# Performance work log

Hardware: AMD Instinct MI355X
Metric: run time of the kernel (lower is better)

The kernel has to match this reference:

```python
import jax, jax.numpy as jnp
import numpy as np
from jax import lax

DN = ('NHWC', 'HWIO', 'NHWC')


def _conv(x, w):
    # x: [B,H,W,Cin], w: [kh,kw,Cin,Cout], 'same' padding
    return lax.conv_general_dilated(x, w, (1, 1), 'SAME', dimension_numbers=DN)


def _hard_sigmoid(x):
    # Keras hard_sigmoid: clip(0.2*x + 0.5, 0, 1)
    return jnp.clip(0.2 * x + 0.5, 0.0, 1.0)


def convlstm2d(x, Wk, Uk, b, filters):
    """Keras ConvLSTM2D, return_sequences=True, padding='same'.
    x: [B,T,H,W,Cin]. Gate order in kernel: [i, f, c, o].
    Returns h sequence [B,T,H,W,filters].
    """
    B, T, H, W, _ = x.shape
    h0 = jnp.zeros((B, H, W, filters), x.dtype)
    c0 = jnp.zeros((B, H, W, filters), x.dtype)

    def step(carry, xt):
        h, c = carry
        z = _conv(xt, Wk) + _conv(h, Uk) + b  # [B,H,W,4*filters]
        zi, zf, zc, zo = jnp.split(z, 4, axis=-1)
        i = _hard_sigmoid(zi)
        f = _hard_sigmoid(zf)
        o = _hard_sigmoid(zo)
        c_new = f * c + i * jnp.tanh(zc)
        h_new = o * jnp.tanh(c_new)
        return (h_new, c_new), h_new

    xs = jnp.moveaxis(x, 1, 0)  # [T,B,H,W,Cin]
    _, hs = lax.scan(step, (h0, c0), xs)
    return jnp.moveaxis(hs, 0, 1)  # [B,T,H,W,filters]


def setup_inputs() -> dict:
    key = jax.random.key(0)
    ks = jax.random.split(key, 7)
    B, T, H, W, Cin, F = 8, 10, 64, 64, 32, 64
    s = 0.05
    return {
        'x': jax.random.normal(ks[0], (B, T, H, W, Cin), jnp.float32),
        'Wk1': jax.random.normal(ks[1], (5, 5, Cin, 4 * F), jnp.float32) * s,
        'Uk1': jax.random.normal(ks[2], (5, 5, F, 4 * F), jnp.float32) * s,
        'b1': jnp.zeros((4 * F,), jnp.float32),
        'Wk2': jax.random.normal(ks[3], (3, 3, F, 4 * F), jnp.float32) * s,
        'Uk2': jax.random.normal(ks[4], (3, 3, F, 4 * F), jnp.float32) * s,
        'b2': jnp.zeros((4 * F,), jnp.float32),
    }


def reference(x, Wk1, Uk1, b1, Wk2, Uk2, b2):
    F = Uk1.shape[2]
    y = jax.nn.relu(convlstm2d(x, Wk1, Uk1, b1, F))
    y = jax.nn.relu(convlstm2d(y, Wk2, Uk2, b2, F))
    return y
```

## Files before the change

### kernel.cpp

```cpp
#include <hip/hip_runtime.h>
#include <cstdint>
#include <cmath>


#define NT        256
#define NTU       256

typedef __attribute__((ext_vector_type(8))) short short8;
typedef __attribute__((ext_vector_type(4))) float f32x4;

__device__ __forceinline__ float hsig(float v) {
    return fminf(fmaxf(fmaf(v, 0.2f, 0.5f), 0.0f), 1.0f);
}

__device__ __forceinline__ short bf16rnd(float f) {
    union { float f; unsigned u; } a; a.f = f;
    return (short)((a.u + 0x7FFFu + ((a.u >> 16) & 1u)) >> 16);
}

__device__ __forceinline__ void split_bf16(float f, short& h, short& l) {
    h = bf16rnd(f);
    union { unsigned u; float f; } b; b.u = ((unsigned)(unsigned short)h) << 16;
    l = bf16rnd(f - b.f);
}

__device__ __forceinline__ float from_bf16(short s) {
    union { unsigned u; float f; } b; b.u = ((unsigned)(unsigned short)s) << 16;
    return b.f;
}

struct BF { uint4 bh[4]; uint4 bl[4]; };

template<int CINX, int KS, bool WRITE_SEQ, bool HZ>
__device__ __forceinline__ void step_body(
    short* __restrict__ xs, short* __restrict__ hs,
    const short* __restrict__ xp, long xp_bstride,
    const short* __restrict__ h_prev,
    float* __restrict__ c_state,
    const short* __restrict__ Wpk,
    const short* __restrict__ Upk,
    const float* __restrict__ bias,
    short* __restrict__ h_next,
    short* __restrict__ seq, long seq_bstride,
    float* __restrict__ outf, long outf_bs,
    int bidx)
{
    constexpr int PAD  = KS / 2;
    constexpr int COLS = 64 + 2 * PAD;
    constexpr int CHX  = CINX / 32;
    constexpr int SEGS = HZ ? CHX : (CHX + 2);
    constexpr int PSTX = 2 * CINX + 8;
    constexpr int PSTH = 136;
    constexpr int VPPX = CINX / 4;

    const int tid  = threadIdx.x;
    const int lane = tid & 63;
    const int fg   = tid >> 6;
    const int q8   = ((lane >> 4) & 3) * 8;
    const int batch = bidx >> 6;
    const int y     = bidx & 63;

    const short* xim = xp + (size_t)batch * xp_bstride;
    const short* him = h_prev + (size_t)batch * 4096 * 128;

    for (int idx = tid; idx < (COLS * PSTX) / 8; idx += NT) {
        uint4 z; z.x = 0; z.y = 0; z.z = 0; z.w = 0;
        *(uint4*)(xs + idx * 8) = z;
    }
    if constexpr (!HZ) {
        for (int idx = tid; idx < (COLS * PSTH) / 8; idx += NT) {
            uint4 z; z.x = 0; z.y = 0; z.z = 0; z.w = 0;
            *(uint4*)(hs + idx * 8) = z;
        }
    }

    f32x4 acc[4][4];
    #pragma unroll
    for (int g = 0; g < 4; ++g)
        #pragma unroll
        for (int mt = 0; mt < 4; ++mt)
            #pragma unroll
            for (int r = 0; r < 4; ++r) acc[g][mt][r] = 0.0f;

    auto loadB = [&](int ky, int kx, int s) -> BF {
        int tap = ky * KS + kx;
        const short* base;
        if (s < CHX)
            base = Wpk + ((size_t)((tap * CHX + s) * 16 + fg)) * 1024 + lane * 16;
        else
            base = Upk + ((size_t)((tap * 2 + (s - CHX)) * 16 + fg)) * 1024 + lane * 16;
        BF b;
        #pragma unroll
        for (int g = 0; g < 4; ++g) {
            b.bh[g] = *(const uint4*)(base + (size_t)g * 4096);
            b.bl[g] = *(const uint4*)(base + (size_t)g * 4096 + 8);
        }
        return b;
    };

    const int ky0   = (y < PAD) ? (PAD - y) : 0;
    const int kyend = (64 + PAD - y) < KS ? (64 + PAD - y) : KS;

    BF bcur = loadB(ky0, 0, 0);

    for (int ky = ky0; ky < kyend; ++ky) {
        int yin = y + ky - PAD;
        __syncthreads();
        const short* xrow = xim + (size_t)yin * 64 * 2 * CINX;
        for (int idx = tid; idx < 64 * VPPX; idx += NT) {
            int px = idx / VPPX;
            int v  = idx - px * VPPX;
            *(uint4*)(xs + (px + PAD) * PSTX + v * 8)
                = *(const uint4*)(xrow + px * 2 * CINX + v * 8);
        }
        if constexpr (!HZ) {
            const short* hrow = him + (size_t)yin * 64 * 128;
            for (int idx = tid; idx < 64 * 16; idx += NT) {
                int px = idx >> 4;
                int v  = idx & 15;
                *(uint4*)(hs + (px + PAD) * PSTH + v * 8)
                    = *(const uint4*)(hrow + px * 128 + v * 8);
            }
        }
        __syncthreads();

        #pragma unroll
        for (int kx = 0; kx < KS; ++kx) {
            #pragma unroll
            for (int s = 0; s < SEGS; ++s) {
                int ns = s + 1, nkx = kx, nky = ky;
                if (ns == SEGS) { ns = 0; ++nkx; }
                if (nkx == KS)  { nkx = 0; ++nky; }
                nky = (nky < kyend) ? nky : ky;
                BF bnxt = loadB(nky, nkx, ns);

                short8 ah[4], al[4];
                #pragma unroll
                for (int mt = 0; mt < 4; ++mt) {
                    int col = mt * 16 + (lane & 15) + kx;
                    const short* p = (s < CHX)
                        ? (xs + col * PSTX + s * 32 + q8)
                        : (hs + col * PSTH + (s - CHX) * 32 + q8);
                    int lo = (s < CHX) ? CINX : 64;
                    ah[mt] = *(const short8*)p;
                    al[mt] = *(const short8*)(p + lo);
                }
                #pragma unroll
                for (int g = 0; g < 4; ++g) {
                    short8 bh = *(const short8*)&bcur.bh[g];
                    short8 bl = *(const short8*)&bcur.bl[g];
                    #pragma unroll
                    for (int mt = 0; mt < 4; ++mt) {
                        acc[g][mt] = __builtin_amdgcn_mfma_f32_16x16x32_bf16(
                            ah[mt], bh, acc[g][mt], 0, 0, 0);
                        acc[g][mt] = __builtin_amdgcn_mfma_f32_16x16x32_bf16(
                            al[mt], bh, acc[g][mt], 0, 0, 0);
                        acc[g][mt] = __builtin_amdgcn_mfma_f32_16x16x32_bf16(
                            ah[mt], bl, acc[g][mt], 0, 0, 0);
                    }
                }
                bcur = bnxt;
            }
        }
    }

    const int fl = fg * 16 + (lane & 15);
    const float b_i = bias[fl];
    const float b_f = bias[64 + fl];
    const float b_c = bias[128 + fl];
    const float b_o = bias[192 + fl];
    const int q = (lane >> 4) & 3;

    const long pixbase = (long)batch * 4096 + (long)y * 64;
    const long cb = pixbase * 64 + fl;
    const long sb = (long)batch * seq_bstride + ((long)y * 64) * 128 + fl;
    const long ob = (long)batch * outf_bs + ((long)y * 64) * 64 + fl;

    #pragma unroll
    for (int mt = 0; mt < 4; ++mt) {
        #pragma unroll
        for (int r = 0; r < 4; ++r) {
            int col = mt * 16 + q * 4 + r;
            long cidx = cb + (long)col * 64;
            float zi = acc[0][mt][r] + b_i;
            float zf = acc[1][mt][r] + b_f;
            float zc = acc[2][mt][r] + b_c;
            float zo = acc[3][mt][r] + b_o;
            float ig = hsig(zi);
            float fgt = hsig(zf);
            float og = hsig(zo);
            float cp = HZ ? 0.0f : c_state[cidx];
            float cn = fgt * cp + ig * tanhf(zc);
            float hn = og * tanhf(cn);
            c_state[cidx] = cn;

            if (h_next) {
                short hh, hl;
                split_bf16(hn, hh, hl);
                long hoff = (pixbase + col) * 128 + fl;
                h_next[hoff]      = hh;
                h_next[hoff + 64] = hl;
            }
            if (WRITE_SEQ) {
                short hh, hl;
                split_bf16(hn, hh, hl);
                bool pos = hn > 0.0f;
                seq[sb + (long)col * 128]      = pos ? hh : (short)0;
                seq[sb + (long)col * 128 + 64] = pos ? hl : (short)0;
            }
            if (outf)
                outf[ob + (long)col * 64] = fmaxf(hn, 0.0f);
        }
    }
}

template<int CINX, int KS, bool WRITE_SEQ, bool HZ>
__global__ __launch_bounds__(NT, 2)
void convlstm_step(
    const short* __restrict__ xp, long xp_bstride,
    const short* __restrict__ h_prev,
    float* __restrict__ c_state,
    const short* __restrict__ Wpk,
    const short* __restrict__ Upk,
    const float* __restrict__ bias,
    short* __restrict__ h_next,
    short* __restrict__ seq, long seq_bstride,
    float* __restrict__ outf, long outf_bs)
{
    extern __shared__ __align__(16) short smem[];
    constexpr int PAD  = KS / 2;
    constexpr int COLS = 64 + 2 * PAD;
    constexpr int PSTX = 2 * CINX + 8;
    step_body<CINX, KS, WRITE_SEQ, HZ>(
        smem, smem + COLS * PSTX,
        xp, xp_bstride, h_prev, c_state, Wpk, Upk, bias,
        h_next, seq, seq_bstride, outf, outf_bs, (int)blockIdx.x);
}

__global__ __launch_bounds__(NT, 3)
void convlstm_fused(
    const short* __restrict__ x1, long x1_bs,
    const short* __restrict__ h1p, float* __restrict__ c1,
    const short* __restrict__ Wp1, const short* __restrict__ Up1,
    const float* __restrict__ b1,
    short* __restrict__ h1n, short* __restrict__ seq1, long seq1_bs,
    const short* __restrict__ x2, long x2_bs,
    const short* __restrict__ h2p, float* __restrict__ c2,
    const short* __restrict__ Wp2, const short* __restrict__ Up2,
    const float* __restrict__ b2,
    short* __restrict__ h2n,
    float* __restrict__ outf2, long outf2_bs)
{
    extern __shared__ __align__(16) short smem[];
    const int b = (int)blockIdx.x;
    if (b < 512) {
        step_body<32, 5, true, false>(
            smem, smem + 68 * 72,
            x1, x1_bs, h1p, c1, Wp1, Up1, b1, h1n, seq1, seq1_bs,
            nullptr, 0, b);
    } else {
        step_body<64, 3, false, false>(
            smem, smem + 66 * 136,
            x2, x2_bs, h2p, c2, Wp2, Up2, b2, h2n, nullptr, 0,
            outf2, outf2_bs, b - 512);
    }
}

__global__ void convert_planes32(const float4* __restrict__ src,
                                 unsigned* __restrict__ dst, int n4)
{
    int t = blockIdx.x * NTU + threadIdx.x;
    if (t >= n4) return;
    int pix = t >> 3;
    int c4  = t & 7;
    float4 v = src[t];
    short h0, l0, h1, l1, h2, l2, h3, l3;
    split_bf16(v.x, h0, l0);
    split_bf16(v.y, h1, l1);
    split_bf16(v.z, h2, l2);
    split_bf16(v.w, h3, l3);
    unsigned* p = dst + (size_t)pix * 32;
    p[c4 * 2]      = (unsigned)(unsigned short)h0 | ((unsigned)(unsigned short)h1 << 16);
    p[c4 * 2 + 1]  = (unsigned)(unsigned short)h2 | ((unsigned)(unsigned short)h3 << 16);
    p[16 + c4 * 2]     = (unsigned)(unsigned short)l0 | ((unsigned)(unsigned short)l1 << 16);
    p[16 + c4 * 2 + 1] = (unsigned)(unsigned short)l2 | ((unsigned)(unsigned short)l3 << 16);
}

__global__ void repack(const float* __restrict__ src, short* __restrict__ dst,
                       int KS, int CH)
{
    int total = KS * KS * CH * 16 * 64;
    int t = blockIdx.x * NTU + threadIdx.x;
    if (t >= total) return;
    int u = t >> 6, lane = t & 63;
    int tap = u / (CH * 16);
    int rem = u - tap * (CH * 16);
    int ch = rem >> 4;
    int gfg = rem & 15;
    int g = gfg >> 2, fgp = gfg & 3;
    int CIN = CH * 32;
    int n = lane & 15, qq = lane >> 4;
    short* d = dst + (size_t)u * 1024 + lane * 16;
    int gc = g * 64 + fgp * 16 + n;
    for (int j = 0; j < 8; ++j) {
        int c = ch * 32 + qq * 8 + j;
        float w = src[((size_t)tap * CIN + c) * 256 + gc];
        short h, l;
        split_bf16(w, h, l);
        d[j] = h;
        d[8 + j] = l;
    }
}

__global__ void relu_copy(const short* __restrict__ hp, float* __restrict__ out,
                          long out_bstride)
{
    long i = (long)blockIdx.x * NTU + threadIdx.x;
    long pix = i >> 6;
    int c = (int)(i & 63);
    float f = from_bf16(hp[pix * 128 + c]) + from_bf16(hp[pix * 128 + 64 + c]);
    long b = pix >> 12;
    long within = (pix & 4095) * 64 + c;
    out[b * out_bstride + within] = fmaxf(f, 0.0f);
}

extern "C" void kernel_launch(void* const* d_in, const int* in_sizes, int n_in,
                              void* d_out, int out_size, void* d_ws, size_t ws_size,
                              hipStream_t stream) {
    const float* x   = (const float*)d_in[0];
    const float* Wk1 = (const float*)d_in[1];
    const float* Uk1 = (const float*)d_in[2];
    const float* b1  = (const float*)d_in[3];
    const float* Wk2 = (const float*)d_in[4];
    const float* Uk2 = (const float*)d_in[5];
    const float* b2  = (const float*)d_in[6];
    float* out = (float*)d_out;

    const long S  = (long)8 * 64 * 64 * 64;
    const long oT = (long)64 * 64 * 64;
    const long oB = 10 * oT;
    const long x1T = (long)4096 * 64;
    const long x1B = 10 * x1T;
    const long sqB = (long)4096 * 128;

    const size_t HB  = (size_t)4 * S;
    const size_t CB  = (size_t)4 * S;
    const size_t W1B = (size_t)25 * 1 * 16 * 1024 * 2;
    const size_t U1B = (size_t)25 * 2 * 16 * 1024 * 2;
    const size_t W2B = (size_t)9 * 2 * 16 * 1024 * 2;
    const size_t U2B = (size_t)9 * 2 * 16 * 1024 * 2;
    const size_t XPB = (size_t)8 * x1B * 2;
    const size_t need_ov = 6 * HB + 2 * CB + W1B + U1B + W2B + U2B + XPB;
    const bool ov = (ws_size >= need_ov);

    short* h1a = (short*)d_ws;
    short* h1b = h1a + 2 * S;
    short *h2a, *h2b;
    float *c1, *c2;
    short* Wp1;
    if (ov) {
        h2a = h1b + 2 * S;
        h2b = h2a + 2 * S;
        c1  = (float*)(h2b + 2 * S);
        c2  = c1 + S;
        Wp1 = (short*)(c2 + S);
    } else {
        h2a = h1a; h2b = h1b;
        c1  = (float*)(h1b + 2 * S);
        c2  = c1;
        Wp1 = (short*)(c1 + S);
    }
    short* Up1 = Wp1 + 25 * 1 * 16 * 1024;
    short* Wp2 = Up1 + 25 * 2 * 16 * 1024;
    short* Up2 = Wp2 + 9 * 2 * 16 * 1024;
    short* x1p = Up2 + 9 * 2 * 16 * 1024;
    short* sqA = x1p + 8 * x1B;
    short* sqB_ = sqA + 2 * S;

    {
        int n4 = 8 * 10 * 4096 * 8;
        convert_planes32<<<dim3((n4 + NTU - 1) / NTU), dim3(NTU), 0, stream>>>(
            (const float4*)x, (unsigned*)x1p, n4);
    }
    repack<<<dim3((25 * 1 * 16 * 64 + NTU - 1) / NTU), dim3(NTU), 0, stream>>>(Wk1, Wp1, 5, 1);
    repack<<<dim3((25 * 2 * 16 * 64 + NTU - 1) / NTU), dim3(NTU), 0, stream>>>(Uk1, Up1, 5, 2);
    repack<<<dim3((9 * 2 * 16 * 64 + NTU - 1) / NTU), dim3(NTU), 0, stream>>>(Wk2, Wp2, 3, 2);
    repack<<<dim3((9 * 2 * 16 * 64 + NTU - 1) / NTU), dim3(NTU), 0, stream>>>(Uk2, Up2, 3, 2);

    const size_t SH_L1HZ = (size_t)(68 * 72) * 2;
    const size_t SH_L1   = (size_t)(68 * 72 + 68 * 136) * 2;
    const size_t SH_L2   = (size_t)(66 * 136) * 4;
    const size_t SH_F    = SH_L2;

    if (ov) {
        hipMemsetAsync(h2a, 0, HB, stream);
        hipMemsetAsync(c2, 0, CB, stream);

        convlstm_step<32, 5, true, true><<<dim3(512), dim3(NT), SH_L1HZ, stream>>>(
            x1p, x1B, h1a, c1, Wp1, Up1, b1, h1b, sqA, sqB,
            nullptr, 0);

        short* hc1 = h1b; short* hn1 = h1a;
        short* hc2 = h2a; short* hn2 = h2b;
        for (int t = 1; t < 10; ++t) {
            short* seq_w = (t & 1) ? sqB_ : sqA;
            short* seq_r = (t & 1) ? sqA : sqB_;
            convlstm_fused<<<dim3(1024), dim3(NT), SH_F, stream>>>(
                x1p + (size_t)t * x1T, x1B, hc1, c1, Wp1, Up1, b1, hn1,
                seq_w, sqB,
                seq_r, sqB, hc2, c2, Wp2, Up2, b2, hn2,
                out + (size_t)(t - 1) * oT, oB);
            short* tmp;
            tmp = hc1; hc1 = hn1; hn1 = tmp;
            tmp = hc2; hc2 = hn2; hn2 = tmp;
        }
        convlstm_step<64, 3, false, false><<<dim3(512), dim3(NT), SH_L2, stream>>>(
            sqB_, sqB, hc2, c2, Wp2, Up2, b2, nullptr,
            nullptr, 0, out + (size_t)9 * oT, oB);
    } else {
        short* seqs = (short*)d_out;
        convlstm_step<32, 5, true, true><<<dim3(512), dim3(NT), SH_L1HZ, stream>>>(
            x1p, x1B, h1a, c1, Wp1, Up1, b1, h1b, seqs, oB * 2,
            nullptr, 0);
        short* hc = h1b; short* hn = h1a;
        for (int t = 1; t < 10; ++t) {
            convlstm_step<32, 5, true, false><<<dim3(512), dim3(NT), SH_L1, stream>>>(
                x1p + (size_t)t * x1T, x1B, hc, c1, Wp1, Up1, b1, hn,
                seqs + (size_t)t * oT * 2, oB * 2, nullptr, 0);
            short* tmp = hc; hc = hn; hn = tmp;
        }
        hipMemsetAsync(hc, 0, HB, stream);
        hipMemsetAsync(c2, 0, CB, stream);
        convlstm_step<64, 3, false, false><<<dim3(512), dim3(NT), SH_L2, stream>>>(
            seqs, oB * 2, hc, c2, Wp2, Up2, b2, hn, nullptr, 0,
            nullptr, 0);
        relu_copy<<<dim3(8192), dim3(NTU), 0, stream>>>(hn, out, oB);
        { short* tmp = hc; hc = hn; hn = tmp; }
        for (int t = 1; t < 10; ++t) {
            convlstm_step<64, 3, false, false><<<dim3(512), dim3(NT), SH_L2, stream>>>(
                seqs + (size_t)t * oT * 2, oB * 2, hc, c2, Wp2, Up2, b2, hn,
                nullptr, 0, nullptr, 0);
            relu_copy<<<dim3(8192), dim3(NTU), 0, stream>>>(hn, out + (size_t)t * oT, oB);
            short* tmp = hc; hc = hn; hn = tmp;
        }
    }
}
```

Measured before the change: 1.650 ms.

## Split each output row into two 32-column halves per block

Each block now computes half a row (32 pixels) instead of a full 64-pixel row, which doubles the grid to 1024 blocks per layer-step (2048 in the fused kernel). Shared memory per block shrinks to the narrower halo span, and launch bounds on the fused kernel are raised so more blocks fit per CU. The aim is better occupancy and load balance on a device with many CUs. In exchange, every weight fragment loaded from global memory now feeds half as many MFMAs, and each half reloads the halo columns, so weight and L2 traffic roughly doubles.

```diff
diff --git a/kernel.cpp b/kernel.cpp
--- a/kernel.cpp
+++ b/kernel.cpp
@@ -43,10 +43,11 @@
     short* __restrict__ h_next,
     short* __restrict__ seq, long seq_bstride,
     float* __restrict__ outf, long outf_bs,
-    int bidx)
+    int unit)
 {
     constexpr int PAD  = KS / 2;
-    constexpr int COLS = 64 + 2 * PAD;
+    constexpr int SPAN = 32 + 2 * PAD;
+    constexpr int MTN  = 2;
     constexpr int CHX  = CINX / 32;
     constexpr int SEGS = HZ ? CHX : (CHX + 2);
     constexpr int PSTX = 2 * CINX + 8;
@@ -57,28 +58,29 @@
     const int lane = tid & 63;
     const int fg   = tid >> 6;
     const int q8   = ((lane >> 4) & 3) * 8;
-    const int batch = bidx >> 6;
-    const int y     = bidx & 63;
+    const int batch = unit >> 7;
+    const int y     = (unit & 127) >> 1;
+    const int col0  = (unit & 1) * 32;
 
     const short* xim = xp + (size_t)batch * xp_bstride;
     const short* him = h_prev + (size_t)batch * 4096 * 128;
 
-    for (int idx = tid; idx < (COLS * PSTX) / 8; idx += NT) {
+    for (int idx = tid; idx < (SPAN * PSTX) / 8; idx += NT) {
         uint4 z; z.x = 0; z.y = 0; z.z = 0; z.w = 0;
         *(uint4*)(xs + idx * 8) = z;
     }
     if constexpr (!HZ) {
-        for (int idx = tid; idx < (COLS * PSTH) / 8; idx += NT) {
+        for (int idx = tid; idx < (SPAN * PSTH) / 8; idx += NT) {
             uint4 z; z.x = 0; z.y = 0; z.z = 0; z.w = 0;
             *(uint4*)(hs + idx * 8) = z;
         }
     }
 
-    f32x4 acc[4][4];
+    f32x4 acc[4][MTN];
     #pragma unroll
     for (int g = 0; g < 4; ++g)
         #pragma unroll
-        for (int mt = 0; mt < 4; ++mt)
+        for (int mt = 0; mt < MTN; ++mt)
             #pragma unroll
             for (int r = 0; r < 4; ++r) acc[g][mt][r] = 0.0f;
 
@@ -107,19 +109,23 @@
         int yin = y + ky - PAD;
         __syncthreads();
         const short* xrow = xim + (size_t)yin * 64 * 2 * CINX;
-        for (int idx = tid; idx < 64 * VPPX; idx += NT) {
+        for (int idx = tid; idx < SPAN * VPPX; idx += NT) {
             int px = idx / VPPX;
             int v  = idx - px * VPPX;
-            *(uint4*)(xs + (px + PAD) * PSTX + v * 8)
-                = *(const uint4*)(xrow + px * 2 * CINX + v * 8);
+            int gc = col0 - PAD + px;
+            if (gc >= 0 && gc < 64)
+                *(uint4*)(xs + px * PSTX + v * 8)
+                    = *(const uint4*)(xrow + gc * 2 * CINX + v * 8);
         }
         if constexpr (!HZ) {
             const short* hrow = him + (size_t)yin * 64 * 128;
-            for (int idx = tid; idx < 64 * 16; idx += NT) {
+            for (int idx = tid; idx < SPAN * 16; idx += NT) {
                 int px = idx >> 4;
                 int v  = idx & 15;
-                *(uint4*)(hs + (px + PAD) * PSTH + v * 8)
-                    = *(const uint4*)(hrow + px * 128 + v * 8);
+                int gc = col0 - PAD + px;
+                if (gc >= 0 && gc < 64)
+                    *(uint4*)(hs + px * PSTH + v * 8)
+                        = *(const uint4*)(hrow + gc * 128 + v * 8);
             }
         }
         __syncthreads();
@@ -134,13 +140,13 @@
                 nky = (nky < kyend) ? nky : ky;
                 BF bnxt = loadB(nky, nkx, ns);
 
-                short8 ah[4], al[4];
+                short8 ah[MTN], al[MTN];
                 #pragma unroll
-                for (int mt = 0; mt < 4; ++mt) {
-                    int col = mt * 16 + (lane & 15) + kx;
+                for (int mt = 0; mt < MTN; ++mt) {
+                    int wc = mt * 16 + (lane & 15) + kx;
                     const short* p = (s < CHX)
-                        ? (xs + col * PSTX + s * 32 + q8)
-                        : (hs + col * PSTH + (s - CHX) * 32 + q8);
+                        ? (xs + wc * PSTX + s * 32 + q8)
+                        : (hs + wc * PSTH + (s - CHX) * 32 + q8);
                     int lo = (s < CHX) ? CINX : 64;
                     ah[mt] = *(const short8*)p;
                     al[mt] = *(const short8*)(p + lo);
@@ -150,7 +156,7 @@
                     short8 bh = *(const short8*)&bcur.bh[g];
                     short8 bl = *(const short8*)&bcur.bl[g];
                     #pragma unroll
-                    for (int mt = 0; mt < 4; ++mt) {
+                    for (int mt = 0; mt < MTN; ++mt) {
                         acc[g][mt] = __builtin_amdgcn_mfma_f32_16x16x32_bf16(
                             ah[mt], bh, acc[g][mt], 0, 0, 0);
                         acc[g][mt] = __builtin_amdgcn_mfma_f32_16x16x32_bf16(
@@ -177,10 +183,10 @@
     const long ob = (long)batch * outf_bs + ((long)y * 64) * 64 + fl;
 
     #pragma unroll
-    for (int mt = 0; mt < 4; ++mt) {
+    for (int mt = 0; mt < MTN; ++mt) {
         #pragma unroll
         for (int r = 0; r < 4; ++r) {
-            int col = mt * 16 + q * 4 + r;
+            int col = col0 + mt * 16 + q * 4 + r;
             long cidx = cb + (long)col * 64;
             float zi = acc[0][mt][r] + b_i;
             float zf = acc[1][mt][r] + b_f;
@@ -229,15 +235,15 @@
 {
     extern __shared__ __align__(16) short smem[];
     constexpr int PAD  = KS / 2;
-    constexpr int COLS = 64 + 2 * PAD;
+    constexpr int SPAN = 32 + 2 * PAD;
     constexpr int PSTX = 2 * CINX + 8;
     step_body<CINX, KS, WRITE_SEQ, HZ>(
-        smem, smem + COLS * PSTX,
+        smem, smem + SPAN * PSTX,
         xp, xp_bstride, h_prev, c_state, Wpk, Upk, bias,
         h_next, seq, seq_bstride, outf, outf_bs, (int)blockIdx.x);
 }
 
-__global__ __launch_bounds__(NT, 3)
+__global__ __launch_bounds__(NT, 4)
 void convlstm_fused(
     const short* __restrict__ x1, long x1_bs,
     const short* __restrict__ h1p, float* __restrict__ c1,
@@ -253,16 +259,16 @@
 {
     extern __shared__ __align__(16) short smem[];
     const int b = (int)blockIdx.x;
-    if (b < 512) {
+    if (b < 1024) {
         step_body<32, 5, true, false>(
-            smem, smem + 68 * 72,
+            smem, smem + 36 * 72,
             x1, x1_bs, h1p, c1, Wp1, Up1, b1, h1n, seq1, seq1_bs,
             nullptr, 0, b);
     } else {
         step_body<64, 3, false, false>(
-            smem, smem + 66 * 136,
+            smem, smem + 34 * 136,
             x2, x2_bs, h2p, c2, Wp2, Up2, b2, h2n, nullptr, 0,
-            outf2, outf2_bs, b - 512);
+            outf2, outf2_bs, b - 1024);
     }
 }
 
@@ -387,16 +393,16 @@
     repack<<<dim3((9 * 2 * 16 * 64 + NTU - 1) / NTU), dim3(NTU), 0, stream>>>(Wk2, Wp2, 3, 2);
     repack<<<dim3((9 * 2 * 16 * 64 + NTU - 1) / NTU), dim3(NTU), 0, stream>>>(Uk2, Up2, 3, 2);
 
-    const size_t SH_L1HZ = (size_t)(68 * 72) * 2;
-    const size_t SH_L1   = (size_t)(68 * 72 + 68 * 136) * 2;
-    const size_t SH_L2   = (size_t)(66 * 136) * 4;
+    const size_t SH_L1HZ = (size_t)(36 * 72) * 2;
+    const size_t SH_L1   = (size_t)(36 * 72 + 36 * 136) * 2;
+    const size_t SH_L2   = (size_t)(34 * 136) * 4;
     const size_t SH_F    = SH_L2;
 
     if (ov) {
         hipMemsetAsync(h2a, 0, HB, stream);
         hipMemsetAsync(c2, 0, CB, stream);
 
-        convlstm_step<32, 5, true, true><<<dim3(512), dim3(NT), SH_L1HZ, stream>>>(
+        convlstm_step<32, 5, true, true><<<dim3(1024), dim3(NT), SH_L1HZ, stream>>>(
             x1p, x1B, h1a, c1, Wp1, Up1, b1, h1b, sqA, sqB,
             nullptr, 0);
 
@@ -405,7 +411,7 @@
         for (int t = 1; t < 10; ++t) {
             short* seq_w = (t & 1) ? sqB_ : sqA;
             short* seq_r = (t & 1) ? sqA : sqB_;
-            convlstm_fused<<<dim3(1024), dim3(NT), SH_F, stream>>>(
+            convlstm_fused<<<dim3(2048), dim3(NT), SH_F, stream>>>(
                 x1p + (size_t)t * x1T, x1B, hc1, c1, Wp1, Up1, b1, hn1,
                 seq_w, sqB,
                 seq_r, sqB, hc2, c2, Wp2, Up2, b2, hn2,
@@ -414,30 +420,30 @@
             tmp = hc1; hc1 = hn1; hn1 = tmp;
             tmp = hc2; hc2 = hn2; hn2 = tmp;
         }
-        convlstm_step<64, 3, false, false><<<dim3(512), dim3(NT), SH_L2, stream>>>(
+        convlstm_step<64, 3, false, false><<<dim3(1024), dim3(NT), SH_L2, stream>>>(
             sqB_, sqB, hc2, c2, Wp2, Up2, b2, nullptr,
             nullptr, 0, out + (size_t)9 * oT, oB);
     } else {
         short* seqs = (short*)d_out;
-        convlstm_step<32, 5, true, true><<<dim3(512), dim3(NT), SH_L1HZ, stream>>>(
+        convlstm_step<32, 5, true, true><<<dim3(1024), dim3(NT), SH_L1HZ, stream>>>(
             x1p, x1B, h1a, c1, Wp1, Up1, b1, h1b, seqs, oB * 2,
             nullptr, 0);
         short* hc = h1b; short* hn = h1a;
         for (int t = 1; t < 10; ++t) {
-            convlstm_step<32, 5, true, false><<<dim3(512), dim3(NT), SH_L1, stream>>>(
+            convlstm_step<32, 5, true, false><<<dim3(1024), dim3(NT), SH_L1, stream>>>(
                 x1p + (size_t)t * x1T, x1B, hc, c1, Wp1, Up1, b1, hn,
                 seqs + (size_t)t * oT * 2, oB * 2, nullptr, 0);
             short* tmp = hc; hc = hn; hn = tmp;
         }
         hipMemsetAsync(hc, 0, HB, stream);
         hipMemsetAsync(c2, 0, CB, stream);
-        convlstm_step<64, 3, false, false><<<dim3(512), dim3(NT), SH_L2, stream>>>(
+        convlstm_step<64, 3, false, false><<<dim3(1024), dim3(NT), SH_L2, stream>>>(
             seqs, oB * 2, hc, c2, Wp2, Up2, b2, hn, nullptr, 0,
             nullptr, 0);
         relu_copy<<<dim3(8192), dim3(NTU), 0, stream>>>(hn, out, oB);
         { short* tmp = hc; hc = hn; hn = tmp; }
         for (int t = 1; t < 10; ++t) {
-            convlstm_step<64, 3, false, false><<<dim3(512), dim3(NT), SH_L2, stream>>>(
+            convlstm_step<64, 3, false, false><<<dim3(1024), dim3(NT), SH_L2, stream>>>(
                 seqs + (size_t)t * oT * 2, oB * 2, hc, c2, Wp2, Up2, b2, hn,
                 nullptr, 0, nullptr, 0);
             relu_copy<<<dim3(8192), dim3(NTU), 0, stream>>>(hn, out + (size_t)t * oT, oB);
```

Result: slower. 1.861 ms (+12.8%).

## Prefetch B fragments per gate instead of per segment to cut registers

Applied to the files above, without the earlier changes.

Replaces the full per-segment B-fragment double buffer (eight uint4 registers for the next segment) with a per-gate rolling prefetch that loads only the next gate's high and low fragments. This shrinks register pressure, and launch bounds are raised from three to four blocks per SIMD to exploit it. s_setprio is also raised around each MFMA group to favour matrix issue. The shorter prefetch distance gives less time to hide global/L2 load latency behind the MFMAs, and the tighter register cap may cause spills.

```diff
diff --git a/kernel.cpp b/kernel.cpp
--- a/kernel.cpp
+++ b/kernel.cpp
@@ -29,7 +29,7 @@
     return b.f;
 }
 
-struct BF { uint4 bh[4]; uint4 bl[4]; };
+struct BG { uint4 h, l; };
 
 template<int CINX, int KS, bool WRITE_SEQ, bool HZ>
 __device__ __forceinline__ void step_body(
@@ -82,26 +82,25 @@
             #pragma unroll
             for (int r = 0; r < 4; ++r) acc[g][mt][r] = 0.0f;
 
-    auto loadB = [&](int ky, int kx, int s) -> BF {
+    const int foff = fg * 1024 + lane * 16;
+    auto bptr = [&](int ky, int kx, int s) -> const short* {
         int tap = ky * KS + kx;
-        const short* base;
-        if (s < CHX)
-            base = Wpk + ((size_t)((tap * CHX + s) * 16 + fg)) * 1024 + lane * 16;
-        else
-            base = Upk + ((size_t)((tap * 2 + (s - CHX)) * 16 + fg)) * 1024 + lane * 16;
-        BF b;
-        #pragma unroll
-        for (int g = 0; g < 4; ++g) {
-            b.bh[g] = *(const uint4*)(base + (size_t)g * 4096);
-            b.bl[g] = *(const uint4*)(base + (size_t)g * 4096 + 8);
-        }
+        return (s < CHX)
+            ? Wpk + (size_t)(tap * CHX + s) * 16384 + foff
+            : Upk + (size_t)(tap * 2 + (s - CHX)) * 16384 + foff;
+    };
+    auto loadG = [&](const short* base, int g) -> BG {
+        BG b;
+        b.h = *(const uint4*)(base + (size_t)g * 4096);
+        b.l = *(const uint4*)(base + (size_t)g * 4096 + 8);
         return b;
     };
 
     const int ky0   = (y < PAD) ? (PAD - y) : 0;
     const int kyend = (64 + PAD - y) < KS ? (64 + PAD - y) : KS;
 
-    BF bcur = loadB(ky0, 0, 0);
+    const short* curb = bptr(ky0, 0, 0);
+    BG bg = loadG(curb, 0);
 
     for (int ky = ky0; ky < kyend; ++ky) {
         int yin = y + ky - PAD;
@@ -132,7 +131,7 @@
                 if (ns == SEGS) { ns = 0; ++nkx; }
                 if (nkx == KS)  { nkx = 0; ++nky; }
                 nky = (nky < kyend) ? nky : ky;
-                BF bnxt = loadB(nky, nkx, ns);
+                const short* nxtb = bptr(nky, nkx, ns);
 
                 short8 ah[4], al[4];
                 #pragma unroll
@@ -147,8 +146,10 @@
                 }
                 #pragma unroll
                 for (int g = 0; g < 4; ++g) {
-                    short8 bh = *(const short8*)&bcur.bh[g];
-                    short8 bl = *(const short8*)&bcur.bl[g];
+                    BG bn = (g < 3) ? loadG(curb, g + 1) : loadG(nxtb, 0);
+                    short8 bh = *(const short8*)&bg.h;
+                    short8 bl = *(const short8*)&bg.l;
+                    __builtin_amdgcn_s_setprio(1);
                     #pragma unroll
                     for (int mt = 0; mt < 4; ++mt) {
                         acc[g][mt] = __builtin_amdgcn_mfma_f32_16x16x32_bf16(
@@ -158,8 +159,10 @@
                         acc[g][mt] = __builtin_amdgcn_mfma_f32_16x16x32_bf16(
                             ah[mt], bl, acc[g][mt], 0, 0, 0);
                     }
+                    __builtin_amdgcn_s_setprio(0);
+                    bg = bn;
                 }
-                bcur = bnxt;
+                curb = nxtb;
             }
         }
     }
@@ -237,7 +240,7 @@
         h_next, seq, seq_bstride, outf, outf_bs, (int)blockIdx.x);
 }
 
-__global__ __launch_bounds__(NT, 3)
+__global__ __launch_bounds__(NT, 4)
 void convlstm_fused(
     const short* __restrict__ x1, long x1_bs,
     const short* __restrict__ h1p, float* __restrict__ c1,
```

Result: slower. 1.959 ms (+18.7%).

## Load conv input rows via global_load_lds and double-buffer h rows in LDS

Applied to the files above, without the earlier changes.

Pads global h and x layouts to the LDS row stride (136/72 shorts) so rows can be copied directly with global_load_lds 16-byte transfers, bypassing registers. Layer-1 h rows are double-buffered so the next row's load is issued before the current row's MFMA work. This is meant to hide row-load latency and cut VGPR traffic. In exchange it uses more shared memory per block (the fused kernel now reserves the larger layer-1 size), which may lower occupancy, and it adds padded buffers.

```diff
diff --git a/kernel.cpp b/kernel.cpp
--- a/kernel.cpp
+++ b/kernel.cpp
@@ -29,11 +29,18 @@
     return b.f;
 }
 
+__device__ __forceinline__ void glds16(const short* g, short* l) {
+    __builtin_amdgcn_global_load_lds(
+        (const __attribute__((address_space(1))) void*)g,
+        (__attribute__((address_space(3))) void*)l,
+        16, 0, 0);
+}
+
 struct BF { uint4 bh[4]; uint4 bl[4]; };
 
-template<int CINX, int KS, bool WRITE_SEQ, bool HZ>
+template<int CINX, int KS, bool WRITE_SEQ, bool HZ, bool XGLDS, bool HDBUF>
 __device__ __forceinline__ void step_body(
-    short* __restrict__ xs, short* __restrict__ hs,
+    short* __restrict__ smem,
     const short* __restrict__ xp, long xp_bstride,
     const short* __restrict__ h_prev,
     float* __restrict__ c_state,
@@ -51,7 +58,12 @@
     constexpr int SEGS = HZ ? CHX : (CHX + 2);
     constexpr int PSTX = 2 * CINX + 8;
     constexpr int PSTH = 136;
-    constexpr int VPPX = CINX / 4;
+    constexpr int XCH  = 64 * (PSTX / 8);
+    constexpr int HCH  = 64 * (PSTH / 8);
+
+    short* xs  = smem;
+    short* hs0 = smem + COLS * PSTX;
+    short* hs1 = HDBUF ? (hs0 + COLS * PSTH) : hs0;
 
     const int tid  = threadIdx.x;
     const int lane = tid & 63;
@@ -61,16 +73,14 @@
     const int y     = bidx & 63;
 
     const short* xim = xp + (size_t)batch * xp_bstride;
-    const short* him = h_prev + (size_t)batch * 4096 * 128;
-
-    for (int idx = tid; idx < (COLS * PSTX) / 8; idx += NT) {
-        uint4 z; z.x = 0; z.y = 0; z.z = 0; z.w = 0;
-        *(uint4*)(xs + idx * 8) = z;
-    }
-    if constexpr (!HZ) {
-        for (int idx = tid; idx < (COLS * PSTH) / 8; idx += NT) {
+    const short* him = h_prev + (size_t)batch * 4096 * PSTH;
+
+    {
+        constexpr int TOT = COLS * PSTX
+            + (HZ ? 0 : (HDBUF ? 2 : 1) * COLS * PSTH);
+        for (int idx = tid; idx < TOT / 8; idx += NT) {
             uint4 z; z.x = 0; z.y = 0; z.z = 0; z.w = 0;
-            *(uint4*)(hs + idx * 8) = z;
+            *(uint4*)(smem + idx * 8) = z;
         }
     }
 
@@ -103,26 +113,44 @@
 
     BF bcur = loadB(ky0, 0, 0);
 
+    short* hrd = hs0;
+    short* hwr = hs1;
+    if constexpr (!HZ && HDBUF) {
+        __syncthreads();
+        const short* hrow = him + (size_t)(y + ky0 - PAD) * 64 * PSTH;
+        for (int idx = tid; idx < HCH; idx += NT)
+            glds16(hrow + idx * 8, hrd + PAD * PSTH + idx * 8);
+    }
+
     for (int ky = ky0; ky < kyend; ++ky) {
         int yin = y + ky - PAD;
         __syncthreads();
-        const short* xrow = xim + (size_t)yin * 64 * 2 * CINX;
-        for (int idx = tid; idx < 64 * VPPX; idx += NT) {
-            int px = idx / VPPX;
-            int v  = idx - px * VPPX;
-            *(uint4*)(xs + (px + PAD) * PSTX + v * 8)
-                = *(const uint4*)(xrow + px * 2 * CINX + v * 8);
-        }
-        if constexpr (!HZ) {
-            const short* hrow = him + (size_t)yin * 64 * 128;
+        if constexpr (XGLDS) {
+            const short* xrow = xim + (size_t)yin * 64 * PSTX;
+            for (int idx = tid; idx < XCH; idx += NT)
+                glds16(xrow + idx * 8, xs + PAD * PSTX + idx * 8);
+        } else {
+            const short* xrow = xim + (size_t)yin * 64 * 128;
             for (int idx = tid; idx < 64 * 16; idx += NT) {
                 int px = idx >> 4;
                 int v  = idx & 15;
-                *(uint4*)(hs + (px + PAD) * PSTH + v * 8)
-                    = *(const uint4*)(hrow + px * 128 + v * 8);
+                *(uint4*)(xs + (px + PAD) * PSTX + v * 8)
+                    = *(const uint4*)(xrow + px * 128 + v * 8);
             }
         }
+        if constexpr (!HZ && !HDBUF) {
+            const short* hrow = him + (size_t)yin * 64 * PSTH;
+            for (int idx = tid; idx < HCH; idx += NT)
+                glds16(hrow + idx * 8, hs0 + PAD * PSTH + idx * 8);
+        }
         __syncthreads();
+        if constexpr (!HZ && HDBUF) {
+            if (ky + 1 < kyend) {
+                const short* hrow = him + (size_t)(yin + 1) * 64 * PSTH;
+                for (int idx = tid; idx < HCH; idx += NT)
+                    glds16(hrow + idx * 8, hwr + PAD * PSTH + idx * 8);
+            }
+        }
 
         #pragma unroll
         for (int kx = 0; kx < KS; ++kx) {
@@ -140,7 +168,7 @@
                     int col = mt * 16 + (lane & 15) + kx;
                     const short* p = (s < CHX)
                         ? (xs + col * PSTX + s * 32 + q8)
-                        : (hs + col * PSTH + (s - CHX) * 32 + q8);
+                        : (hrd + col * PSTH + (s - CHX) * 32 + q8);
                     int lo = (s < CHX) ? CINX : 64;
                     ah[mt] = *(const short8*)p;
                     al[mt] = *(const short8*)(p + lo);
@@ -162,6 +190,7 @@
                 bcur = bnxt;
             }
         }
+        if constexpr (HDBUF) { short* t = hrd; hrd = hwr; hwr = t; }
     }
 
     const int fl = fg * 16 + (lane & 15);
@@ -197,7 +226,7 @@
             if (h_next) {
                 short hh, hl;
                 split_bf16(hn, hh, hl);
-                long hoff = (pixbase + col) * 128 + fl;
+                long hoff = (pixbase + col) * 136 + fl;
                 h_next[hoff]      = hh;
                 h_next[hoff + 64] = hl;
             }
@@ -214,7 +243,7 @@
     }
 }
 
-template<int CINX, int KS, bool WRITE_SEQ, bool HZ>
+template<int CINX, int KS, bool WRITE_SEQ, bool HZ, bool XGLDS, bool HDBUF>
 __global__ __launch_bounds__(NT, 2)
 void convlstm_step(
     const short* __restrict__ xp, long xp_bstride,
@@ -228,12 +257,8 @@
     float* __restrict__ outf, long outf_bs)
 {
     extern __shared__ __align__(16) short smem[];
-    constexpr int PAD  = KS / 2;
-    constexpr int COLS = 64 + 2 * PAD;
-    constexpr int PSTX = 2 * CINX + 8;
-    step_body<CINX, KS, WRITE_SEQ, HZ>(
-        smem, smem + COLS * PSTX,
-        xp, xp_bstride, h_prev, c_state, Wpk, Upk, bias,
+    step_body<CINX, KS, WRITE_SEQ, HZ, XGLDS, HDBUF>(
+        smem, xp, xp_bstride, h_prev, c_state, Wpk, Upk, bias,
         h_next, seq, seq_bstride, outf, outf_bs, (int)blockIdx.x);
 }
 
@@ -254,14 +279,12 @@
     extern __shared__ __align__(16) short smem[];
     const int b = (int)blockIdx.x;
     if (b < 512) {
-        step_body<32, 5, true, false>(
-            smem, smem + 68 * 72,
-            x1, x1_bs, h1p, c1, Wp1, Up1, b1, h1n, seq1, seq1_bs,
+        step_body<32, 5, true, false, true, true>(
+            smem, x1, x1_bs, h1p, c1, Wp1, Up1, b1, h1n, seq1, seq1_bs,
             nullptr, 0, b);
     } else {
-        step_body<64, 3, false, false>(
-            smem, smem + 66 * 136,
-            x2, x2_bs, h2p, c2, Wp2, Up2, b2, h2n, nullptr, 0,
+        step_body<64, 3, false, false, false, false>(
+            smem, x2, x2_bs, h2p, c2, Wp2, Up2, b2, h2n, nullptr, 0,
             outf2, outf2_bs, b - 512);
     }
 }
@@ -279,7 +302,7 @@
     split_bf16(v.y, h1, l1);
     split_bf16(v.z, h2, l2);
     split_bf16(v.w, h3, l3);
-    unsigned* p = dst + (size_t)pix * 32;
+    unsigned* p = dst + (size_t)pix * 36;
     p[c4 * 2]      = (unsigned)(unsigned short)h0 | ((unsigned)(unsigned short)h1 << 16);
     p[c4 * 2 + 1]  = (unsigned)(unsigned short)h2 | ((unsigned)(unsigned short)h3 << 16);
     p[16 + c4 * 2]     = (unsigned)(unsigned short)l0 | ((unsigned)(unsigned short)l1 << 16);
@@ -318,7 +341,7 @@
     long i = (long)blockIdx.x * NTU + threadIdx.x;
     long pix = i >> 6;
     int c = (int)(i & 63);
-    float f = from_bf16(hp[pix * 128 + c]) + from_bf16(hp[pix * 128 + 64 + c]);
+    float f = from_bf16(hp[pix * 136 + c]) + from_bf16(hp[pix * 136 + 64 + c]);
     long b = pix >> 12;
     long within = (pix & 4095) * 64 + c;
     out[b * out_bstride + within] = fmaxf(f, 0.0f);
@@ -339,34 +362,38 @@
     const long S  = (long)8 * 64 * 64 * 64;
     const long oT = (long)64 * 64 * 64;
     const long oB = 10 * oT;
-    const long x1T = (long)4096 * 64;
+    const long x1T = (long)4096 * 72;
     const long x1B = 10 * x1T;
     const long sqB = (long)4096 * 128;
-
-    const size_t HB  = (size_t)4 * S;
+    const long HSH = (long)8 * 4096 * 136;
+    const long SQSH = (long)8 * 4096 * 128;
+
+    const size_t HB  = (size_t)HSH * 2;
     const size_t CB  = (size_t)4 * S;
     const size_t W1B = (size_t)25 * 1 * 16 * 1024 * 2;
     const size_t U1B = (size_t)25 * 2 * 16 * 1024 * 2;
     const size_t W2B = (size_t)9 * 2 * 16 * 1024 * 2;
     const size_t U2B = (size_t)9 * 2 * 16 * 1024 * 2;
     const size_t XPB = (size_t)8 * x1B * 2;
-    const size_t need_ov = 6 * HB + 2 * CB + W1B + U1B + W2B + U2B + XPB;
+    const size_t SQB2 = (size_t)SQSH * 2;
+    const size_t need_ov = 4 * HB + 2 * CB + W1B + U1B + W2B + U2B + XPB
+                         + 2 * SQB2;
     const bool ov = (ws_size >= need_ov);
 
     short* h1a = (short*)d_ws;
-    short* h1b = h1a + 2 * S;
+    short* h1b = h1a + HSH;
     short *h2a, *h2b;
     float *c1, *c2;
     short* Wp1;
     if (ov) {
-        h2a = h1b + 2 * S;
-        h2b = h2a + 2 * S;
-        c1  = (float*)(h2b + 2 * S);
+        h2a = h1b + HSH;
+        h2b = h2a + HSH;
+        c1  = (float*)(h2b + HSH);
         c2  = c1 + S;
         Wp1 = (short*)(c2 + S);
     } else {
         h2a = h1a; h2b = h1b;
-        c1  = (float*)(h1b + 2 * S);
+        c1  = (float*)(h1b + HSH);
         c2  = c1;
         Wp1 = (short*)(c1 + S);
     }
@@ -375,7 +402,7 @@
     short* Up2 = Wp2 + 9 * 2 * 16 * 1024;
     short* x1p = Up2 + 9 * 2 * 16 * 1024;
     short* sqA = x1p + 8 * x1B;
-    short* sqB_ = sqA + 2 * S;
+    short* sqBuf = sqA + SQSH;
 
     {
         int n4 = 8 * 10 * 4096 * 8;
@@ -388,23 +415,23 @@
     repack<<<dim3((9 * 2 * 16 * 64 + NTU - 1) / NTU), dim3(NTU), 0, stream>>>(Uk2, Up2, 3, 2);
 
     const size_t SH_L1HZ = (size_t)(68 * 72) * 2;
-    const size_t SH_L1   = (size_t)(68 * 72 + 68 * 136) * 2;
-    const size_t SH_L2   = (size_t)(66 * 136) * 4;
-    const size_t SH_F    = SH_L2;
+    const size_t SH_L1   = (size_t)(68 * 72 + 2 * 68 * 136) * 2;
+    const size_t SH_L2   = (size_t)(66 * 136 * 2) * 2;
+    const size_t SH_F    = SH_L1;
 
     if (ov) {
         hipMemsetAsync(h2a, 0, HB, stream);
         hipMemsetAsync(c2, 0, CB, stream);
 
-        convlstm_step<32, 5, true, true><<<dim3(512), dim3(NT), SH_L1HZ, stream>>>(
-            x1p, x1B, h1a, c1, Wp1, Up1, b1, h1b, sqA, sqB,
-            nullptr, 0);
+        convlstm_step<32, 5, true, true, true, false>
+            <<<dim3(512), dim3(NT), SH_L1HZ, stream>>>(
+            x1p, x1B, h1a, c1, Wp1, Up1, b1, h1b, sqA, sqB, nullptr, 0);
 
         short* hc1 = h1b; short* hn1 = h1a;
         short* hc2 = h2a; short* hn2 = h2b;
         for (int t = 1; t < 10; ++t) {
-            short* seq_w = (t & 1) ? sqB_ : sqA;
-            short* seq_r = (t & 1) ? sqA : sqB_;
+            short* seq_w = (t & 1) ? sqBuf : sqA;
+            short* seq_r = (t & 1) ? sqA : sqBuf;
             convlstm_fused<<<dim3(1024), dim3(NT), SH_F, stream>>>(
                 x1p + (size_t)t * x1T, x1B, hc1, c1, Wp1, Up1, b1, hn1,
                 seq_w, sqB,
@@ -414,30 +441,33 @@
             tmp = hc1; hc1 = hn1; hn1 = tmp;
             tmp = hc2; hc2 = hn2; hn2 = tmp;
         }
-        convlstm_step<64, 3, false, false><<<dim3(512), dim3(NT), SH_L2, stream>>>(
-            sqB_, sqB, hc2, c2, Wp2, Up2, b2, nullptr,
+        convlstm_step<64, 3, false, false, false, false>
+            <<<dim3(512), dim3(NT), SH_L2, stream>>>(
+            sqBuf, sqB, hc2, c2, Wp2, Up2, b2, nullptr,
             nullptr, 0, out + (size_t)9 * oT, oB);
     } else {
         short* seqs = (short*)d_out;
-        convlstm_step<32, 5, true, true><<<dim3(512), dim3(NT), SH_L1HZ, stream>>>(
-            x1p, x1B, h1a, c1, Wp1, Up1, b1, h1b, seqs, oB * 2,
-            nullptr, 0);
+        convlstm_step<32, 5, true, true, true, false>
+            <<<dim3(512), dim3(NT), SH_L1HZ, stream>>>(
+            x1p, x1B, h1a, c1, Wp1, Up1, b1, h1b, seqs, oB * 2, nullptr, 0);
         short* hc = h1b; short* hn = h1a;
         for (int t = 1; t < 10; ++t) {
-            convlstm_step<32, 5, true, false><<<dim3(512), dim3(NT), SH_L1, stream>>>(
+            convlstm_step<32, 5, true, false, true, true>
+                <<<dim3(512), dim3(NT), SH_L1, stream>>>(
                 x1p + (size_t)t * x1T, x1B, hc, c1, Wp1, Up1, b1, hn,
                 seqs + (size_t)t * oT * 2, oB * 2, nullptr, 0);
             short* tmp = hc; hc = hn; hn = tmp;
         }
         hipMemsetAsync(hc, 0, HB, stream);
         hipMemsetAsync(c2, 0, CB, stream);
-        convlstm_step<64, 3, false, false><<<dim3(512), dim3(NT), SH_L2, stream>>>(
-            seqs, oB * 2, hc, c2, Wp2, Up2, b2, hn, nullptr, 0,
-            nullptr, 0);
+        convlstm_step<64, 3, false, false, false, false>
+            <<<dim3(512), dim3(NT), SH_L2, stream>>>(
+            seqs, oB * 2, hc, c2, Wp2, Up2, b2, hn, nullptr, 0, nullptr, 0);
         relu_copy<<<dim3(8192), dim3(NTU), 0, stream>>>(hn, out, oB);
         { short* tmp = hc; hc = hn; hn = tmp; }
         for (int t = 1; t < 10; ++t) {
-            convlstm_step<64, 3, false, false><<<dim3(512), dim3(NT), SH_L2, stream>>>(
+            convlstm_step<64, 3, false, false, false, false>
+                <<<dim3(512), dim3(NT), SH_L2, stream>>>(
                 seqs + (size_t)t * oT * 2, oB * 2, hc, c2, Wp2, Up2, b2, hn,
                 nullptr, 0, nullptr, 0);
             relu_copy<<<dim3(8192), dim3(NTU), 0, stream>>>(hn, out + (size_t)t * oT, oB);
```

Result: no change. 1.652 ms (+0.1%).
